# Kernel tuning notes

Measured on AMD Instinct MI355X. Metric: run time of the kernel, lower is better.

Reference implementation:

```python
import jax, jax.numpy as jnp
import numpy as np

N = 100000   # nodes
D = 64       # in_features == out_features
E = 1600000  # edges (avg degree 16)
C = 1.0      # curvature
MIN_NORM = 1e-15
PROJ_EPS = 1e-5
ATANH_CLIP = 1.0 - 1e-7


def _artanh(x):
    return jnp.arctanh(jnp.clip(x, -ATANH_CLIP, ATANH_CLIP))


def _norm(x):
    return jnp.clip(jnp.linalg.norm(x, axis=-1, keepdims=True), MIN_NORM)


def setup_inputs() -> dict:
    key = jax.random.key(0)
    k1, k2, k3, k4, k5 = jax.random.split(key, 5)
    # points inside the unit ball (module assumes input already on manifold)
    x = 0.05 * jax.random.normal(k1, (N, D), dtype=jnp.float32)
    # xavier_uniform with gain sqrt(2): std ~= sqrt(2)*sqrt(2/(D+D))
    W = jax.random.normal(k2, (D, D), dtype=jnp.float32) * np.float32(np.sqrt(4.0 / (2 * D)))
    edge_vals = jax.random.uniform(k3, (E,), dtype=jnp.float32) / 16.0  # ~normalized adjacency
    rows = jax.random.randint(k4, (E,), 0, N, dtype=jnp.int32)
    cols = jax.random.randint(k5, (E,), 0, N, dtype=jnp.int32)
    return {"x": x, "W": W, "edge_vals": edge_vals, "rows": rows, "cols": cols}


def reference(x, W, edge_vals, rows, cols):
    sc = jnp.sqrt(jnp.float32(C))
    # --- Poincare Linear: mobius_matvec(W, x, c) (no bias, eval-mode dropout) ---
    mx = x @ W.T                                  # [N, D]
    x_n = _norm(x)
    mx_n = _norm(mx)
    res = jnp.tanh(mx_n / x_n * _artanh(sc * x_n)) * mx / (mx_n * sc)
    res = jnp.where(jnp.all(mx == 0, axis=-1, keepdims=True), 0.0, res)
    # --- poincare2euclidean == logmap0 ---
    p_n = _norm(res)
    hidden = _artanh(sc * p_n) * res / (sc * p_n)  # tangent at origin
    # --- sparse adjacency matmul: support = adj @ hidden ---
    gathered = edge_vals[:, None] * hidden[cols]   # [E, D]
    support = jax.ops.segment_sum(gathered, rows, num_segments=N)
    # --- euclidean2poincare == expmap0 ---
    u_n = _norm(support)
    p = jnp.tanh(sc * u_n) * support / (sc * u_n)
    # --- Act: relu(logmap0) -> proj_tan0 (identity) -> expmap0 -> proj ---
    pn2 = _norm(p)
    xt = jax.nn.relu(_artanh(sc * pn2) * p / (sc * pn2))
    xt_n = _norm(xt)
    out = jnp.tanh(sc * xt_n) * xt / (sc * xt_n)
    o_n = _norm(out)
    max_n = (1.0 - PROJ_EPS) / sc
    out = jnp.where(o_n > max_n, out / o_n * max_n, out)
    return out
```

## Files before the change

kernel.cpp:

```cpp
#include <hip/hip_runtime.h>
#include <hip/hip_fp16.h>

#define NN 100000
#define DD 64
#define EE 1600000
#define NB 512
#define NPB 196
#define CHUNK 3125
#define CAP 3520

typedef _Float16 half8 __attribute__((ext_vector_type(8)));
typedef float floatx4 __attribute__((ext_vector_type(4)));

__device__ __forceinline__ float frcp(float x) { return __builtin_amdgcn_rcpf(x); }

__device__ __forceinline__ float fast_tanh(float x) {
    float t = __expf(2.0f * x);
    return (t - 1.0f) * frcp(t + 1.0f);
}
__device__ __forceinline__ float fast_atanh(float x) {
    const float CLIP = 1.0f - 1e-7f;
    x = fminf(fmaxf(x, -CLIP), CLIP);
    return 0.5f * __logf((1.0f + x) * frcp(1.0f - x));
}
__device__ __forceinline__ float group16_reduce_sum(float v) {
    #pragma unroll
    for (int m = 8; m > 0; m >>= 1) v += __shfl_xor(v, m, 16);
    return v;
}
__device__ __forceinline__ float lo16f(unsigned u) {
    return __half2float(__ushort_as_half((unsigned short)(u & 0xFFFFu)));
}
__device__ __forceinline__ float hi16f(unsigned u) {
    return __half2float(__ushort_as_half((unsigned short)(u >> 16)));
}

__global__ __launch_bounds__(1024) void linear_count_kernel(
    const float* __restrict__ x, const float* __restrict__ W,
    const int* __restrict__ rows,
    __half* __restrict__ hidden, int* __restrict__ cnt) {
    __shared__ _Float16 Wh[64 * 80];
    __shared__ int h[NB];
    const int t = threadIdx.x;

    if (t < NB) h[t] = 0;
    for (int i = t; i < 64 * 64; i += 1024)
        Wh[(i >> 6) * 80 + (i & 63)] = (_Float16)W[i];
    __syncthreads();

    {
        const int e0 = blockIdx.x * CHUNK;
        for (int i = t; i < CHUNK; i += 1024)
            atomicAdd(&h[(unsigned)rows[e0 + i] / NPB], 1);
    }

    const int lane = t & 63;
    const int wv   = t >> 6;
    if (wv < 13) {
        const int q    = lane >> 4;
        const int c    = lane & 15;
        const int node = blockIdx.x * NPB + wv * 16 + c;
        const int node_ld = (node < NN) ? node : (NN - 1);

        const float MIN_NORM = 1e-15f;
        const float4* xr = (const float4*)(x + node_ld * 64);
        float4 b0a = xr[q * 2];
        float4 b0b = xr[q * 2 + 1];
        float4 b1a = xr[8 + q * 2];
        float4 b1b = xr[8 + q * 2 + 1];

        float xpart = b0a.x*b0a.x + b0a.y*b0a.y + b0a.z*b0a.z + b0a.w*b0a.w
                    + b0b.x*b0b.x + b0b.y*b0b.y + b0b.z*b0b.z + b0b.w*b0b.w
                    + b1a.x*b1a.x + b1a.y*b1a.y + b1a.z*b1a.z + b1a.w*b1a.w
                    + b1b.x*b1b.x + b1b.y*b1b.y + b1b.z*b1b.z + b1b.w*b1b.w;
        xpart += __shfl_xor(xpart, 16, 64);
        xpart += __shfl_xor(xpart, 32, 64);
        float x_n = fmaxf(sqrtf(xpart), MIN_NORM);

        half8 bf0, bf1;
        bf0[0]=(_Float16)b0a.x; bf0[1]=(_Float16)b0a.y; bf0[2]=(_Float16)b0a.z; bf0[3]=(_Float16)b0a.w;
        bf0[4]=(_Float16)b0b.x; bf0[5]=(_Float16)b0b.y; bf0[6]=(_Float16)b0b.z; bf0[7]=(_Float16)b0b.w;
        bf1[0]=(_Float16)b1a.x; bf1[1]=(_Float16)b1a.y; bf1[2]=(_Float16)b1a.z; bf1[3]=(_Float16)b1a.w;
        bf1[4]=(_Float16)b1b.x; bf1[5]=(_Float16)b1b.y; bf1[6]=(_Float16)b1b.z; bf1[7]=(_Float16)b1b.w;

        floatx4 acc[4];
        #pragma unroll
        for (int tt = 0; tt < 4; ++tt) {
            const half8* a0 = (const half8*)&Wh[(16 * tt + c) * 80 + q * 8];
            const half8* a1 = (const half8*)&Wh[(16 * tt + c) * 80 + 32 + q * 8];
            floatx4 z = {0.f, 0.f, 0.f, 0.f};
            z = __builtin_amdgcn_mfma_f32_16x16x32_f16(a0[0], bf0, z, 0, 0, 0);
            z = __builtin_amdgcn_mfma_f32_16x16x32_f16(a1[0], bf1, z, 0, 0, 0);
            acc[tt] = z;
        }

        float hscale = fast_atanh(x_n) * frcp(x_n);

        if (node < NN) {
            #pragma unroll
            for (int tt = 0; tt < 4; ++tt) {
                __half2 lo = __floats2half2_rn(acc[tt][0] * hscale, acc[tt][1] * hscale);
                __half2 hi = __floats2half2_rn(acc[tt][2] * hscale, acc[tt][3] * hscale);
                uint2 pkt;
                pkt.x = *(unsigned*)&lo;
                pkt.y = *(unsigned*)&hi;
                ((uint2*)hidden)[node * 16 + tt * 4 + q] = pkt;
            }
        }
    }
    __syncthreads();
    if (t < NB) cnt[blockIdx.x * NB + t] = h[t];
}

__global__ __launch_bounds__(512) void offset_kernel(const int* __restrict__ cnt,
                                                     int* __restrict__ woff,
                                                     int* __restrict__ gcount) {
    const int lane = threadIdx.x & 63;
    const int b    = blockIdx.x * 8 + (threadIdx.x >> 6);
    int c[8]; int sum = 0;
    #pragma unroll
    for (int k = 0; k < 8; ++k) { c[k] = cnt[(lane * 8 + k) * NB + b]; sum += c[k]; }
    int pre = sum;
    #pragma unroll
    for (int m = 1; m < 64; m <<= 1) {
        int u = __shfl_up(pre, m, 64);
        if (lane >= m) pre += u;
    }
    int run = pre - sum;
    #pragma unroll
    for (int k = 0; k < 8; ++k) { woff[(lane * 8 + k) * NB + b] = run; run += c[k]; }
    if (lane == 63) gcount[b] = run;
}

__global__ __launch_bounds__(64) void scan_kernel(const int* __restrict__ gcount,
                                                  int* __restrict__ bbase) {
    const int lane = threadIdx.x;
    int c[8]; int sum = 0;
    #pragma unroll
    for (int k = 0; k < 8; ++k) { c[k] = gcount[lane * 8 + k]; sum += c[k]; }
    int pre = sum;
    #pragma unroll
    for (int m = 1; m < 64; m <<= 1) {
        int u = __shfl_up(pre, m, 64);
        if (lane >= m) pre += u;
    }
    int run = pre - sum;
    #pragma unroll
    for (int k = 0; k < 8; ++k) { bbase[lane * 8 + k] = run; run += c[k]; }
    if (lane == 63) bbase[NB] = run;
}

__global__ __launch_bounds__(1024) void sort_scatter_kernel(
    const int* __restrict__ rows, const int* __restrict__ cols,
    const float* __restrict__ ev, const int* __restrict__ cnt,
    const int* __restrict__ woff, const int* __restrict__ bbase,
    int2* __restrict__ csr) {
    __shared__ int cur[NB];
    __shared__ int delta[NB];
    __shared__ int2 sorted[CHUNK];
    __shared__ unsigned short bid[CHUNK];
    const int t  = threadIdx.x;
    const int e0 = blockIdx.x * CHUNK;

    if (t < 64) {
        const int lane = t;
        int c[8]; int sum = 0;
        #pragma unroll
        for (int k = 0; k < 8; ++k) { c[k] = cnt[blockIdx.x * NB + lane * 8 + k]; sum += c[k]; }
        int pre = sum;
        #pragma unroll
        for (int m = 1; m < 64; m <<= 1) {
            int u = __shfl_up(pre, m, 64);
            if (lane >= m) pre += u;
        }
        int run = pre - sum;
        #pragma unroll
        for (int k = 0; k < 8; ++k) {
            int b = lane * 8 + k;
            cur[b]   = run;
            delta[b] = bbase[b] + woff[blockIdx.x * NB + b] - run;
            run += c[k];
        }
    }
    __syncthreads();
    for (int i = t; i < CHUNK; i += 1024) {
        unsigned r = (unsigned)rows[e0 + i];
        unsigned c = (unsigned)cols[e0 + i];
        float v = ev[e0 + i];
        unsigned b  = r / NPB;
        unsigned rl = r - b * NPB;
        int idx = atomicAdd(&cur[b], 1);
        sorted[idx] = make_int2((int)((rl << 24) | (c << 7)), __float_as_int(v));
        bid[idx] = (unsigned short)b;
    }
    __syncthreads();
    for (int i = t; i < CHUNK; i += 1024) {
        int2 eV = sorted[i];
        csr[delta[bid[i]] + i] = eV;
    }
}

__global__ __launch_bounds__(1024) void sortgather_kernel(
    const __half* __restrict__ hidden, const int2* __restrict__ csr,
    const int* __restrict__ bbase, float* __restrict__ out) {
    __shared__ int2 srt[CAP];
    __shared__ int cnt_a[NPB];
    __shared__ int start[NPB];
    __shared__ int cur[NPB];
    const int t  = threadIdx.x;
    const int b  = blockIdx.x;
    const int lo = bbase[b];
    int cnt = bbase[b + 1] - lo;
    if (cnt > CAP) cnt = CAP;

    if (t < NPB) cnt_a[t] = 0;
    __syncthreads();
    for (int i = t; i < cnt; i += 1024)
        atomicAdd(&cnt_a[((unsigned)csr[lo + i].x) >> 24], 1);
    __syncthreads();
    if (t < 64) {
        const int lane = t;
        int c[4]; int sum = 0;
        #pragma unroll
        for (int k = 0; k < 4; ++k) {
            int bb = lane * 4 + k;
            c[k] = (bb < NPB) ? cnt_a[bb] : 0;
            sum += c[k];
        }
        int pre = sum;
        #pragma unroll
        for (int m = 1; m < 64; m <<= 1) {
            int u = __shfl_up(pre, m, 64);
            if (lane >= m) pre += u;
        }
        int run = pre - sum;
        #pragma unroll
        for (int k = 0; k < 4; ++k) {
            int bb = lane * 4 + k;
            if (bb < NPB) { start[bb] = run; cur[bb] = run; run += c[k]; }
        }
    }
    __syncthreads();
    for (int i = t; i < cnt; i += 1024) {
        int2 e = csr[lo + i];
        int rl = ((unsigned)e.x) >> 24;
        int p  = atomicAdd(&cur[rl], 1);
        srt[p] = e;
    }
    __syncthreads();

    const int lane = t & 63;
    const int wv   = t >> 6;
    const int g    = lane >> 4;
    const int l8   = (lane & 15) * 8;
    const char* __restrict__ hidc = (const char*)hidden;
    const float MIN_NORM = 1e-15f;
    const float MAX_N = 1.0f - 1e-5f;

    for (int n = wv; n < NPB; n += 16) {
        int i   = start[n];
        int rhi = i + cnt_a[n];
        float ax = 0.f, ay = 0.f, az = 0.f, aw = 0.f;

        for (; i + 8 <= rhi; i += 8) {
            int2 dA = srt[i + g];
            int2 dB = srt[i + 4 + g];
            unsigned oA = (((unsigned)dA.x) & 0xFFFFFFu) + l8;
            unsigned oB = (((unsigned)dB.x) & 0xFFFFFFu) + l8;
            uint2 hA = *(const uint2*)(hidc + oA);
            uint2 hB = *(const uint2*)(hidc + oB);
            float vA = __int_as_float(dA.y);
            float vB = __int_as_float(dB.y);
            ax = fmaf(vA, lo16f(hA.x), ax);
            ay = fmaf(vA, hi16f(hA.x), ay);
            az = fmaf(vA, lo16f(hA.y), az);
            aw = fmaf(vA, hi16f(hA.y), aw);
            ax = fmaf(vB, lo16f(hB.x), ax);
            ay = fmaf(vB, hi16f(hB.x), ay);
            az = fmaf(vB, lo16f(hB.y), az);
            aw = fmaf(vB, hi16f(hB.y), aw);
        }
        for (; i < rhi; i += 4) {
            int idx = i + g;
            int2 d = srt[(idx < rhi) ? idx : (rhi - 1)];
            float v = (idx < rhi) ? __int_as_float(d.y) : 0.0f;
            unsigned o = (((unsigned)d.x) & 0xFFFFFFu) + l8;
            uint2 h = *(const uint2*)(hidc + o);
            ax = fmaf(v, lo16f(h.x), ax);
            ay = fmaf(v, hi16f(h.x), ay);
            az = fmaf(v, lo16f(h.y), az);
            aw = fmaf(v, hi16f(h.y), aw);
        }

        ax += __shfl_xor(ax, 16, 64); ax += __shfl_xor(ax, 32, 64);
        ay += __shfl_xor(ay, 16, 64); ay += __shfl_xor(ay, 32, 64);
        az += __shfl_xor(az, 16, 64); az += __shfl_xor(az, 32, 64);
        aw += __shfl_xor(aw, 16, 64); aw += __shfl_xor(aw, 32, 64);

        float xx = fmaxf(ax, 0.f), xy = fmaxf(ay, 0.f);
        float xz = fmaxf(az, 0.f), xw = fmaxf(aw, 0.f);

        float part = xx*xx + xy*xy + xz*xz + xw*xw;
        float xt_n = fmaxf(sqrtf(group16_reduce_sum(part)), MIN_NORM);
        float txt  = fast_tanh(xt_n);
        float s3   = txt * frcp(xt_n);
        if (txt > MAX_N) s3 = MAX_N * frcp(xt_n);
        float ox = xx*s3, oy = xy*s3, oz = xz*s3, ow = xw*s3;

        int gn = b * NPB + n;
        if (g == 0 && gn < NN) {
            float4 o4 = make_float4(ox, oy, oz, ow);
            *(float4*)(out + gn * DD + (lane & 15) * 4) = o4;
        }
    }
}

extern "C" void kernel_launch(void* const* d_in, const int* in_sizes, int n_in,
                              void* d_out, int out_size, void* d_ws, size_t ws_size,
                              hipStream_t stream) {
    const float* x    = (const float*)d_in[0];
    const float* W    = (const float*)d_in[1];
    const float* ev   = (const float*)d_in[2];
    const int*   rows = (const int*)d_in[3];
    const int*   cols = (const int*)d_in[4];
    float* out = (float*)d_out;

    char* ws = (char*)d_ws;
    __half* hidden = (__half*)ws;
    int2*   csr    = (int2*)(ws + 12800000);
    int*    cnt    = (int*)(ws + 25600000);
    int*    woff   = (int*)(ws + 26648576);
    int*    gcount = (int*)(ws + 27697152);
    int*    bbase  = (int*)(ws + 27699200);

    linear_count_kernel<<<NB, 1024, 0, stream>>>(x, W, rows, hidden, cnt);
    offset_kernel<<<NB / 8, 512, 0, stream>>>(cnt, woff, gcount);
    scan_kernel<<<1, 64, 0, stream>>>(gcount, bbase);
    sort_scatter_kernel<<<NB, 1024, 0, stream>>>(rows, cols, ev, cnt, woff, bbase, csr);
    sortgather_kernel<<<NB, 1024, 0, stream>>>(hidden, csr, bbase, out);
}
```

Measured before the change: 147.4 us.

## Fold global scan into consumers, cache CSR edges in LDS, unroll gather by 16

Removes the single-block scan kernel launch by having each sort_scatter and sortgather block redo the 512-entry exclusive scan of gcount itself. sortgather now keeps the edge chunk it loads in a shared 'raw' buffer, so the second pass reads LDS instead of re-reading the CSR from global memory. The gather loop is unrolled to 16 edges per step for more loads in flight, and launch bounds gain an occupancy hint. The cost is redundant scan work in every block and extra LDS use (about 28KB more per block), which could limit occupancy.

```diff
diff --git a/kernel.cpp b/kernel.cpp
--- a/kernel.cpp
+++ b/kernel.cpp
@@ -132,28 +132,10 @@
     if (lane == 63) gcount[b] = run;
 }
 
-__global__ __launch_bounds__(64) void scan_kernel(const int* __restrict__ gcount,
-                                                  int* __restrict__ bbase) {
-    const int lane = threadIdx.x;
-    int c[8]; int sum = 0;
-    #pragma unroll
-    for (int k = 0; k < 8; ++k) { c[k] = gcount[lane * 8 + k]; sum += c[k]; }
-    int pre = sum;
-    #pragma unroll
-    for (int m = 1; m < 64; m <<= 1) {
-        int u = __shfl_up(pre, m, 64);
-        if (lane >= m) pre += u;
-    }
-    int run = pre - sum;
-    #pragma unroll
-    for (int k = 0; k < 8; ++k) { bbase[lane * 8 + k] = run; run += c[k]; }
-    if (lane == 63) bbase[NB] = run;
-}
-
-__global__ __launch_bounds__(1024) void sort_scatter_kernel(
+__global__ __launch_bounds__(1024, 8) void sort_scatter_kernel(
     const int* __restrict__ rows, const int* __restrict__ cols,
     const float* __restrict__ ev, const int* __restrict__ cnt,
-    const int* __restrict__ woff, const int* __restrict__ bbase,
+    const int* __restrict__ woff, const int* __restrict__ gcount,
     int2* __restrict__ csr) {
     __shared__ int cur[NB];
     __shared__ int delta[NB];
@@ -164,6 +146,16 @@
 
     if (t < 64) {
         const int lane = t;
+        int g[8]; int gsum = 0;
+        #pragma unroll
+        for (int k = 0; k < 8; ++k) { g[k] = gcount[lane * 8 + k]; gsum += g[k]; }
+        int gpre = gsum;
+        #pragma unroll
+        for (int m = 1; m < 64; m <<= 1) {
+            int u = __shfl_up(gpre, m, 64);
+            if (lane >= m) gpre += u;
+        }
+        int grun = gpre - gsum;
         int c[8]; int sum = 0;
         #pragma unroll
         for (int k = 0; k < 8; ++k) { c[k] = cnt[blockIdx.x * NB + lane * 8 + k]; sum += c[k]; }
@@ -178,8 +170,9 @@
         for (int k = 0; k < 8; ++k) {
             int b = lane * 8 + k;
             cur[b]   = run;
-            delta[b] = bbase[b] + woff[blockIdx.x * NB + b] - run;
-            run += c[k];
+            delta[b] = grun + woff[blockIdx.x * NB + b] - run;
+            grun += g[k];
+            run  += c[k];
         }
     }
     __syncthreads();
@@ -200,23 +193,47 @@
     }
 }
 
-__global__ __launch_bounds__(1024) void sortgather_kernel(
+__global__ __launch_bounds__(1024, 8) void sortgather_kernel(
     const __half* __restrict__ hidden, const int2* __restrict__ csr,
-    const int* __restrict__ bbase, float* __restrict__ out) {
+    const int* __restrict__ gcount, float* __restrict__ out) {
+    __shared__ int2 raw[CAP];
     __shared__ int2 srt[CAP];
     __shared__ int cnt_a[NPB];
     __shared__ int start[NPB];
     __shared__ int cur[NPB];
+    __shared__ int s_lo, s_cnt;
     const int t  = threadIdx.x;
     const int b  = blockIdx.x;
-    const int lo = bbase[b];
-    int cnt = bbase[b + 1] - lo;
-    if (cnt > CAP) cnt = CAP;
 
     if (t < NPB) cnt_a[t] = 0;
-    __syncthreads();
-    for (int i = t; i < cnt; i += 1024)
-        atomicAdd(&cnt_a[((unsigned)csr[lo + i].x) >> 24], 1);
+    if (t < 64) {
+        int g[8]; int gsum = 0;
+        #pragma unroll
+        for (int k = 0; k < 8; ++k) { g[k] = gcount[t * 8 + k]; gsum += g[k]; }
+        int gpre = gsum;
+        #pragma unroll
+        for (int m = 1; m < 64; m <<= 1) {
+            int u = __shfl_up(gpre, m, 64);
+            if (t >= m) gpre += u;
+        }
+        int run = gpre - gsum;
+        #pragma unroll
+        for (int k = 0; k < 8; ++k) {
+            int bb = t * 8 + k;
+            if (bb == b) { s_lo = run; s_cnt = g[k]; }
+            run += g[k];
+        }
+    }
+    __syncthreads();
+    const int lo  = s_lo;
+    int ecnt = s_cnt;
+    if (ecnt > CAP) ecnt = CAP;
+
+    for (int i = t; i < ecnt; i += 1024) {
+        int2 e = csr[lo + i];
+        raw[i] = e;
+        atomicAdd(&cnt_a[((unsigned)e.x) >> 24], 1);
+    }
     __syncthreads();
     if (t < 64) {
         const int lane = t;
@@ -241,10 +258,9 @@
         }
     }
     __syncthreads();
-    for (int i = t; i < cnt; i += 1024) {
-        int2 e = csr[lo + i];
-        int rl = ((unsigned)e.x) >> 24;
-        int p  = atomicAdd(&cur[rl], 1);
+    for (int i = t; i < ecnt; i += 1024) {
+        int2 e = raw[i];
+        int p  = atomicAdd(&cur[((unsigned)e.x) >> 24], 1);
         srt[p] = e;
     }
     __syncthreads();
@@ -262,7 +278,41 @@
         int rhi = i + cnt_a[n];
         float ax = 0.f, ay = 0.f, az = 0.f, aw = 0.f;
 
-        for (; i + 8 <= rhi; i += 8) {
+        for (; i + 16 <= rhi; i += 16) {
+            int2 dA = srt[i + g];
+            int2 dB = srt[i + 4 + g];
+            int2 dC = srt[i + 8 + g];
+            int2 dD = srt[i + 12 + g];
+            unsigned oA = (((unsigned)dA.x) & 0xFFFFFFu) + l8;
+            unsigned oB = (((unsigned)dB.x) & 0xFFFFFFu) + l8;
+            unsigned oC = (((unsigned)dC.x) & 0xFFFFFFu) + l8;
+            unsigned oD = (((unsigned)dD.x) & 0xFFFFFFu) + l8;
+            uint2 hA = *(const uint2*)(hidc + oA);
+            uint2 hB = *(const uint2*)(hidc + oB);
+            uint2 hC = *(const uint2*)(hidc + oC);
+            uint2 hD = *(const uint2*)(hidc + oD);
+            float vA = __int_as_float(dA.y);
+            float vB = __int_as_float(dB.y);
+            float vC = __int_as_float(dC.y);
+            float vD = __int_as_float(dD.y);
+            ax = fmaf(vA, lo16f(hA.x), ax);
+            ay = fmaf(vA, hi16f(hA.x), ay);
+            az = fmaf(vA, lo16f(hA.y), az);
+            aw = fmaf(vA, hi16f(hA.y), aw);
+            ax = fmaf(vB, lo16f(hB.x), ax);
+            ay = fmaf(vB, hi16f(hB.x), ay);
+            az = fmaf(vB, lo16f(hB.y), az);
+            aw = fmaf(vB, hi16f(hB.y), aw);
+            ax = fmaf(vC, lo16f(hC.x), ax);
+            ay = fmaf(vC, hi16f(hC.x), ay);
+            az = fmaf(vC, lo16f(hC.y), az);
+            aw = fmaf(vC, hi16f(hC.y), aw);
+            ax = fmaf(vD, lo16f(hD.x), ax);
+            ay = fmaf(vD, hi16f(hD.x), ay);
+            az = fmaf(vD, lo16f(hD.y), az);
+            aw = fmaf(vD, hi16f(hD.y), aw);
+        }
+        if (i + 8 <= rhi) {
             int2 dA = srt[i + g];
             int2 dB = srt[i + 4 + g];
             unsigned oA = (((unsigned)dA.x) & 0xFFFFFFu) + l8;
@@ -279,6 +329,7 @@
             ay = fmaf(vB, hi16f(hB.x), ay);
             az = fmaf(vB, lo16f(hB.y), az);
             aw = fmaf(vB, hi16f(hB.y), aw);
+            i += 8;
         }
         for (; i < rhi; i += 4) {
             int idx = i + g;
@@ -331,11 +382,9 @@
     int*    cnt    = (int*)(ws + 25600000);
     int*    woff   = (int*)(ws + 26648576);
     int*    gcount = (int*)(ws + 27697152);
-    int*    bbase  = (int*)(ws + 27699200);
 
     linear_count_kernel<<<NB, 1024, 0, stream>>>(x, W, rows, hidden, cnt);
     offset_kernel<<<NB / 8, 512, 0, stream>>>(cnt, woff, gcount);
-    scan_kernel<<<1, 64, 0, stream>>>(gcount, bbase);
-    sort_scatter_kernel<<<NB, 1024, 0, stream>>>(rows, cols, ev, cnt, woff, bbase, csr);
-    sortgather_kernel<<<NB, 1024, 0, stream>>>(hidden, csr, bbase, out);
-}
+    sort_scatter_kernel<<<NB, 1024, 0, stream>>>(rows, cols, ev, cnt, woff, gcount, csr);
+    sortgather_kernel<<<NB, 1024, 0, stream>>>(hidden, csr, gcount, out);
+}
```

Result: no change. 147.0 us, median of 2 (-0.3%).
